# Performance work log

Hardware: AMD Instinct MI355X
Metric: run time of the kernel (lower is better)

The kernel has to match this reference:

```python
import jax, jax.numpy as jnp
import numpy as np

C = 96          # num_features
G = 3           # deform / weight groups
K = 9           # 3x3 kernel taps
OFF_CH = G * 3 * K  # 81: offset-conv output channels


def conv3x3(x, w, b=None):
    out = jax.lax.conv_general_dilated(
        x, w, window_strides=(1, 1), padding=((1, 1), (1, 1)),
        dimension_numbers=('NCHW', 'OIHW', 'NCHW'))
    if b is not None:
        out = out + b[None, :, None, None]
    return out


def offset_gen(x):
    o1, o2, m = jnp.split(x, 3, axis=1)
    return jnp.concatenate([o1, o2], axis=1), jax.nn.sigmoid(m)


def dcn(x, offset, mask, w, b):
    # Modulated deformable conv (DCNv2): offset = [y-offsets (G*K ch), x-offsets (G*K ch)]
    N, Cx, H, W = x.shape
    Cg = Cx // G
    GK = G * K
    dy = offset[:, :GK].reshape(N, G, K, H, W)
    dx = offset[:, GK:].reshape(N, G, K, H, W)
    m = mask.reshape(N, G, K, H, W)
    ky = (jnp.arange(K) // 3 - 1).astype(x.dtype)
    kx = (jnp.arange(K) % 3 - 1).astype(x.dtype)
    # sampling positions: p = p0 + kernel_offset + learned_offset (stride 1, pad 1)
    py = dy + jnp.arange(H, dtype=x.dtype)[:, None] + ky[:, None, None]   # [N,G,K,H,W]
    px = dx + jnp.arange(W, dtype=x.dtype) + kx[:, None, None]
    y0 = jnp.floor(py)
    x0 = jnp.floor(px)
    xf = x.reshape(N, G, Cg, H * W)
    gather = jax.vmap(jax.vmap(lambda xg, ig: xg[:, ig]))  # ([Cg,HW],[KHW]) -> [Cg,KHW]
    val = jnp.zeros((N, G, Cg, K, H, W), x.dtype)
    for cy, cx in ((y0, x0), (y0, x0 + 1), (y0 + 1, x0), (y0 + 1, x0 + 1)):
        wgt = (1 - jnp.abs(py - cy)) * (1 - jnp.abs(px - cx))
        valid = (cy >= 0) & (cy <= H - 1) & (cx >= 0) & (cx <= W - 1)
        iy = jnp.clip(cy, 0, H - 1).astype(jnp.int32)
        ix = jnp.clip(cx, 0, W - 1).astype(jnp.int32)
        idx = (iy * W + ix).reshape(N, G, K * H * W)
        g = gather(xf, idx).reshape(N, G, Cg, K, H, W)
        val = val + g * (wgt * valid.astype(x.dtype))[:, :, None]
    val = val * m[:, :, None]                       # modulation
    wg = w.reshape(G, Cx // G, Cg, K)               # grouped weight [G, Cout/G, Cin/G, K]
    out = jnp.einsum('ngckhw,gock->ngohw', val, wg).reshape(N, Cx, H, W)
    return out + b[None, :, None, None]


def setup_inputs() -> dict:
    key = jax.random.key(0)
    ks = jax.random.split(key, 16)
    B, H, W = 2, 128, 128
    d = {
        'X1': jax.random.normal(ks[0], (B, C, H, W), jnp.float32),
        'X2': jax.random.normal(ks[1], (B, C, H, W), jnp.float32),
        'w_bot': jax.random.normal(ks[2], (C, 2 * C, 3, 3), jnp.float32) * 0.02,
    }
    for i in range(4):
        d[f'w_off{i+1}'] = jax.random.normal(ks[3 + i], (OFF_CH, C, 3, 3), jnp.float32) * 0.02
        d[f'w_d{i+1}'] = jax.random.normal(ks[7 + i], (C, C // G, 3, 3), jnp.float32) * 0.05
        d[f'b_d{i+1}'] = jax.random.normal(ks[11 + i], (C,), jnp.float32) * 0.01
    return d


def reference(X1, X2, w_bot, w_off1, w_off2, w_off3, w_off4,
              w_d1, b_d1, w_d2, b_d2, w_d3, b_d3, w_d4, b_d4):
    B, Cx, H, W = X1.shape
    # frames: f0 = cat(X1, X1), f1 = cat(X1, X2) along channels, flattened to (B*2, 2C, H, W)
    feat = jnp.stack([jnp.concatenate([X1, X1], axis=1),
                      jnp.concatenate([X1, X2], axis=1)], axis=1)
    feat = feat.reshape(B * 2, 2 * Cx, H, W)
    feat = conv3x3(feat, w_bot)
    for w_off, w_d, b_d in ((w_off1, w_d1, b_d1), (w_off2, w_d2, b_d2),
                            (w_off3, w_d3, b_d3), (w_off4, w_d4, b_d4)):
        off, m = offset_gen(conv3x3(feat, w_off))
        feat = dcn(feat, off, m, w_d, b_d)
    return feat[1:2]


if __name__ == '__main__':
    out = reference(**setup_inputs())
    print(out.shape)
```

## Files before the change

### kernel.cpp

```cpp
#include <hip/hip_runtime.h>

#define HW 16384
#define W_ 128
#define RSB 130

typedef short short8 __attribute__((ext_vector_type(8)));
typedef float f32x4 __attribute__((ext_vector_type(4)));
typedef unsigned short ushort8v __attribute__((ext_vector_type(8)));

__device__ __forceinline__ float b2f(unsigned short u) {
    return __uint_as_float(((unsigned)u) << 16);
}
__device__ __forceinline__ unsigned short f2b(float f) {
    unsigned u = __float_as_uint(f);
    return (unsigned short)((u + 0x7fffu + ((u >> 16) & 1u)) >> 16);
}

__global__ __launch_bounds__(256) void pack_nhwc(const float* __restrict__ X1,
                                                 const float* __restrict__ X2,
                                                 unsigned short* __restrict__ dst) {
    int i = blockIdx.x * 256 + threadIdx.x;
    int p = i & (HW - 1);
    int cb = i >> 14;
    if (cb >= 24) return;
    int ch = cb * 8;
    int y = p >> 7, x = p & 127;
    ushort8v o;
#pragma unroll
    for (int j = 0; j < 8; ++j) {
        int c = ch + j;
        float v = (c < 96) ? X1[c * HW + p] : X2[(c - 96) * HW + p];
        o[j] = f2b(v);
    }
    *(ushort8v*)(dst + (size_t)((y + 1) * RSB + (x + 1)) * 192 + ch) = o;
}

__global__ __launch_bounds__(256) void prep_all(
    const float* __restrict__ w_bot,
    const float* __restrict__ w_off0, const float* __restrict__ w_off1,
    const float* __restrict__ w_off2, const float* __restrict__ w_off3,
    const float* __restrict__ w_d0, const float* __restrict__ w_d1,
    const float* __restrict__ w_d2, const float* __restrict__ w_d3,
    unsigned short* __restrict__ wBbot, unsigned short* __restrict__ wBoff,
    unsigned short* __restrict__ wdB,  unsigned short* __restrict__ in_nhwc,
    unsigned short* __restrict__ featA, unsigned short* __restrict__ featB) {
    const int region = blockIdx.y;
    const int i = blockIdx.x * 256 + threadIdx.x;
    if (region == 0) {
        if (i >= 165888) return;
        int v = i & 7, lane = (i >> 3) & 63, t = i >> 9;
        int kc = t % 6; t /= 6;
        int tap = t % 9, nt = t / 9;
        int oc = nt * 16 + (lane & 15), cin = kc * 32 + (lane >> 4) * 8 + v;
        wBbot[i] = f2b(oc < 96 ? w_bot[(oc * 192 + cin) * 9 + tap] : 0.f);
    } else if (region <= 4) {
        if (i >= 82944) return;
        const float* w = region == 1 ? w_off0 : region == 2 ? w_off1
                       : region == 3 ? w_off2 : w_off3;
        int v = i & 7, lane = (i >> 3) & 63, t = i >> 9;
        int kc = t % 3; t /= 3;
        int tap = t % 9, nt = t / 9;
        int oc = nt * 16 + (lane & 15), cin = kc * 32 + (lane >> 4) * 8 + v;
        wBoff[(region - 1) * 82944 + i] = f2b(oc < 81 ? w[(oc * 96 + cin) * 9 + tap] : 0.f);
    } else if (region <= 8) {
        if (i >= 27648) return;
        const float* w = region == 5 ? w_d0 : region == 6 ? w_d1
                       : region == 7 ? w_d2 : w_d3;
        int v = i & 7, lane = (i >> 3) & 63, t = i >> 9;
        int nt = t & 1; t >>= 1;
        int tap = t % 9, g = t / 9;
        int oc = nt * 16 + (lane & 15), c = (lane >> 4) * 8 + v;
        wdB[(region - 5) * 27648 + i] = f2b(w[((g * 32 + oc) * 32 + c) * 9 + tap]);
    } else {
        if (i >= 516 * 48) return;
        int bp = i / 48, c8 = i % 48;
        int y, x;
        if (bp < 130)      { y = 0;   x = bp; }
        else if (bp < 260) { y = 129; x = bp - 130; }
        else { int t2 = bp - 260; y = 1 + (t2 >> 1); x = (t2 & 1) ? 129 : 0; }
        size_t pix = (size_t)y * RSB + x;
        ushort8v z = {0, 0, 0, 0, 0, 0, 0, 0};
        if (c8 < 24)      *(ushort8v*)(in_nhwc + pix * 192 + c8 * 8) = z;
        else if (c8 < 36) *(ushort8v*)(featA + pix * 96 + (c8 - 24) * 8) = z;
        else              *(ushort8v*)(featB + pix * 96 + (c8 - 36) * 8) = z;
    }
}

template<int KC, bool FLAT_OUT>
__global__ __launch_bounds__(256) void conv_mfma(const unsigned short* __restrict__ in,
                                                 const unsigned short* __restrict__ wB,
                                                 unsigned short* __restrict__ outb) {
    const int CP = KC * 32;
    const int tid = threadIdx.x;
    const int lane = tid & 63;
    const int wid = tid >> 6;
    const int msub = wid & 1, nh = wid >> 1;
    const int pbase = blockIdx.x * 32 + msub * 16;
    const int p = pbase + (lane & 15);
    const int y = p >> 7, x = p & 127;
    const int klane = lane >> 4;
    const unsigned short* arow = in + (size_t)((y + 1) * RSB + (x + 1)) * CP + klane * 8;
    const unsigned short* wb = wB + (size_t)(nh * 3) * 9 * KC * 512 + lane * 8;

    f32x4 acc0 = {0.f, 0.f, 0.f, 0.f};
    f32x4 acc1 = {0.f, 0.f, 0.f, 0.f};
    f32x4 acc2 = {0.f, 0.f, 0.f, 0.f};

#pragma unroll
    for (int tap = 0; tap < 9; ++tap) {
        const unsigned short* at = arow + ((tap / 3 - 1) * RSB + (tap % 3 - 1)) * CP;
#pragma unroll
        for (int kc = 0; kc < KC; ++kc) {
            short8 a  = *(const short8*)(at + kc * 32);
            short8 b0 = *(const short8*)(wb + ((0 * 9 + tap) * KC + kc) * 512);
            short8 b1 = *(const short8*)(wb + ((1 * 9 + tap) * KC + kc) * 512);
            short8 b2 = *(const short8*)(wb + ((2 * 9 + tap) * KC + kc) * 512);
            acc0 = __builtin_amdgcn_mfma_f32_16x16x32_bf16(a, b0, acc0, 0, 0, 0);
            acc1 = __builtin_amdgcn_mfma_f32_16x16x32_bf16(a, b1, acc1, 0, 0, 0);
            acc2 = __builtin_amdgcn_mfma_f32_16x16x32_bf16(a, b2, acc2, 0, 0, 0);
        }
    }

    const int col = lane & 15;
#pragma unroll
    for (int r = 0; r < 4; ++r) {
        int pr = pbase + klane * 4 + r;
        int yy = pr >> 7, xx = pr & 127;
        size_t base = FLAT_OUT ? (size_t)pr * 96
                               : (size_t)((yy + 1) * RSB + (xx + 1)) * 96;
        outb[base + (nh * 3 + 0) * 16 + col] = f2b(acc0[r]);
        outb[base + (nh * 3 + 1) * 16 + col] = f2b(acc1[r]);
        outb[base + (nh * 3 + 2) * 16 + col] = f2b(acc2[r]);
    }
}

__global__ __launch_bounds__(256) void dcn_kernel(const unsigned short* __restrict__ feat,
                                                  const unsigned short* __restrict__ offb,
                                                  const unsigned short* __restrict__ wdB,
                                                  const float* __restrict__ b_d,
                                                  void* __restrict__ outp,
                                                  int last) {
    const int tid = threadIdx.x;
    const int lane = tid & 63;
    const int wv = tid >> 6;
    const int g = blockIdx.y;
    const int pb = ((blockIdx.x & 7) << 5) + (blockIdx.x >> 3);
    const int pbase = pb * 64 + wv * 16;
    const int col = lane & 15, klane = lane >> 4;
    const int p = pbase + col;
    const int y = p >> 7, x = p & 127;
    const int coct = klane * 8;

    const unsigned short* orow = offb + (size_t)p * 96 + g * 9;
    float dyv[9], dxv[9], mrv[9];
#pragma unroll
    for (int k = 0; k < 9; ++k) {
        dyv[k] = b2f(orow[k]);
        dxv[k] = b2f(orow[27 + k]);
        mrv[k] = b2f(orow[54 + k]);
    }

    const unsigned short* fgc = feat + g * 32 + coct;
    const unsigned short* wb = wdB + (size_t)g * 9 * 2 * 512 + lane * 8;

    f32x4 acc0 = {0.f, 0.f, 0.f, 0.f};
    f32x4 acc1 = {0.f, 0.f, 0.f, 0.f};

#pragma unroll
    for (int k = 0; k < 9; ++k) {
        float m = 1.f / (1.f + __expf(-mrv[k]));

        float py = dyv[k] + (float)y + (float)(k / 3 - 1);
        float px = dxv[k] + (float)x + (float)(k % 3 - 1);
        float y0f = floorf(py), x0f = floorf(px);
        float fy = py - y0f, fx = px - x0f;

        float vy0 = (y0f >= 0.f   && y0f <= 127.f) ? 1.f : 0.f;
        float vy1 = (y0f >= -1.f  && y0f <= 126.f) ? 1.f : 0.f;
        float vx0 = (x0f >= 0.f   && x0f <= 127.f) ? 1.f : 0.f;
        float vx1 = (x0f >= -1.f  && x0f <= 126.f) ? 1.f : 0.f;

        int iy0r = (int)y0f, ix0r = (int)x0f;
        int iy0 = min(max(iy0r, 0), 127);
        int iy1 = min(max(iy0r + 1, 0), 127);
        int ix0 = min(max(ix0r, 0), 127);
        int ix1 = min(max(ix0r + 1, 0), 127);

        float w00 = (1.f - fy) * (1.f - fx) * vy0 * vx0 * m;
        float w01 = (1.f - fy) * fx        * vy0 * vx1 * m;
        float w10 = fy        * (1.f - fx) * vy1 * vx0 * m;
        float w11 = fy        * fx         * vy1 * vx1 * m;

        int r00 = (iy0 + 1) * RSB + ix0 + 1, r01 = (iy0 + 1) * RSB + ix1 + 1;
        int r10 = (iy1 + 1) * RSB + ix0 + 1, r11 = (iy1 + 1) * RSB + ix1 + 1;
        ushort8v v00 = *(const ushort8v*)(fgc + (size_t)r00 * 96);
        ushort8v v01 = *(const ushort8v*)(fgc + (size_t)r01 * 96);
        ushort8v v10 = *(const ushort8v*)(fgc + (size_t)r10 * 96);
        ushort8v v11 = *(const ushort8v*)(fgc + (size_t)r11 * 96);

        short8 a;
#pragma unroll
        for (int j = 0; j < 8; ++j) {
            float val = w00 * b2f(v00[j]) + w01 * b2f(v01[j])
                      + w10 * b2f(v10[j]) + w11 * b2f(v11[j]);
            a[j] = (short)f2b(val);
        }
        short8 b0 = *(const short8*)(wb + (k * 2 + 0) * 512);
        short8 b1 = *(const short8*)(wb + (k * 2 + 1) * 512);
        acc0 = __builtin_amdgcn_mfma_f32_16x16x32_bf16(a, b0, acc0, 0, 0, 0);
        acc1 = __builtin_amdgcn_mfma_f32_16x16x32_bf16(a, b1, acc1, 0, 0, 0);
    }

#pragma unroll
    for (int r = 0; r < 4; ++r) {
        int pr = pbase + klane * 4 + r;
        int ch0 = g * 32 + col, ch1 = g * 32 + 16 + col;
        float o0 = acc0[r] + b_d[ch0];
        float o1 = acc1[r] + b_d[ch1];
        if (!last) {
            int yy = pr >> 7, xx = pr & 127;
            unsigned short* fo = (unsigned short*)outp;
            size_t base = (size_t)((yy + 1) * RSB + (xx + 1)) * 96;
            fo[base + ch0] = f2b(o0);
            fo[base + ch1] = f2b(o1);
        } else {
            float* fo = (float*)outp;
            fo[(size_t)ch0 * HW + pr] = o0;
            fo[(size_t)ch1 * HW + pr] = o1;
        }
    }
}

extern "C" void kernel_launch(void* const* d_in, const int* in_sizes, int n_in,
                              void* d_out, int out_size, void* d_ws, size_t ws_size,
                              hipStream_t stream) {
    const float* X1    = (const float*)d_in[0];
    const float* X2    = (const float*)d_in[1];
    const float* w_bot = (const float*)d_in[2];
    const float* w_off[4] = {(const float*)d_in[3], (const float*)d_in[6],
                             (const float*)d_in[9], (const float*)d_in[12]};
    const float* w_d[4]   = {(const float*)d_in[4], (const float*)d_in[7],
                             (const float*)d_in[10], (const float*)d_in[13]};
    const float* b_d[4]   = {(const float*)d_in[5], (const float*)d_in[8],
                             (const float*)d_in[11], (const float*)d_in[14]};

    unsigned short* in_nhwc = (unsigned short*)d_ws;
    unsigned short* featA   = in_nhwc + 3244800;
    unsigned short* featB   = featA + 1622400;
    unsigned short* off_b   = featB + 1622400;
    unsigned short* wBbot   = off_b + 1572864;
    unsigned short* wBoff   = wBbot + 165888;
    unsigned short* wdB     = wBoff + 4 * 82944;

    prep_all<<<dim3(648, 10), 256, 0, stream>>>(
        w_bot, w_off[0], w_off[1], w_off[2], w_off[3],
        w_d[0], w_d[1], w_d[2], w_d[3],
        wBbot, wBoff, wdB, in_nhwc, featA, featB);
    pack_nhwc<<<1536, 256, 0, stream>>>(X1, X2, in_nhwc);
    conv_mfma<6, false><<<512, 256, 0, stream>>>(in_nhwc, wBbot, featA);

    unsigned short* cur = featA;
    unsigned short* nxt = featB;
    for (int it = 0; it < 4; ++it) {
        conv_mfma<3, true><<<512, 256, 0, stream>>>(cur, wBoff + it * 82944, off_b);
        void* outp = (it == 3) ? d_out : (void*)nxt;
        dcn_kernel<<<dim3(256, 3), 256, 0, stream>>>(cur, off_b, wdB + it * 27648,
                                                     b_d[it], outp, it == 3 ? 1 : 0);
        unsigned short* t = cur; cur = nxt; nxt = t;
    }
}
```

Baseline: 144.0 us.

## Fuse offset convolution into deformable conv kernel via shared memory

Merges the per-iteration offset/mask 3x3 convolution into the DCN kernel: each 512-thread block first computes 81 offset channels for its 64 pixels with MFMA into LDS, then performs the deformable sampling and grouped conv for all three groups. This removes one kernel launch per iteration and the global round-trip of the bf16 offset buffer, and keeps offsets in fp32. In exchange, the grid shrinks from 768 to 256 blocks and the 12 DCN sub-tasks are unevenly split across 8 waves, reducing parallelism.

```diff
diff --git a/kernel.cpp b/kernel.cpp
--- a/kernel.cpp
+++ b/kernel.cpp
@@ -134,99 +134,138 @@
     }
 }
 
-__global__ __launch_bounds__(256) void dcn_kernel(const unsigned short* __restrict__ feat,
-                                                  const unsigned short* __restrict__ offb,
-                                                  const unsigned short* __restrict__ wdB,
-                                                  const float* __restrict__ b_d,
-                                                  void* __restrict__ outp,
-                                                  int last) {
+__global__ __launch_bounds__(512) void offdcn_kernel(
+    const unsigned short* __restrict__ feat,
+    const unsigned short* __restrict__ wBoff,
+    const unsigned short* __restrict__ wdB,
+    const float* __restrict__ b_d,
+    void* __restrict__ outp, int last) {
+    __shared__ float s_off[64][97];
+
     const int tid = threadIdx.x;
     const int lane = tid & 63;
-    const int wv = tid >> 6;
-    const int g = blockIdx.y;
+    const int w = tid >> 6;
+    const int col = lane & 15, klane = lane >> 4;
     const int pb = ((blockIdx.x & 7) << 5) + (blockIdx.x >> 3);
-    const int pbase = pb * 64 + wv * 16;
-    const int col = lane & 15, klane = lane >> 4;
-    const int p = pbase + col;
-    const int y = p >> 7, x = p & 127;
-    const int coct = klane * 8;
-
-    const unsigned short* orow = offb + (size_t)p * 96 + g * 9;
-    float dyv[9], dxv[9], mrv[9];
-#pragma unroll
-    for (int k = 0; k < 9; ++k) {
-        dyv[k] = b2f(orow[k]);
-        dxv[k] = b2f(orow[27 + k]);
-        mrv[k] = b2f(orow[54 + k]);
-    }
-
-    const unsigned short* fgc = feat + g * 32 + coct;
-    const unsigned short* wb = wdB + (size_t)g * 9 * 2 * 512 + lane * 8;
-
-    f32x4 acc0 = {0.f, 0.f, 0.f, 0.f};
-    f32x4 acc1 = {0.f, 0.f, 0.f, 0.f};
-
-#pragma unroll
-    for (int k = 0; k < 9; ++k) {
-        float m = 1.f / (1.f + __expf(-mrv[k]));
-
-        float py = dyv[k] + (float)y + (float)(k / 3 - 1);
-        float px = dxv[k] + (float)x + (float)(k % 3 - 1);
-        float y0f = floorf(py), x0f = floorf(px);
-        float fy = py - y0f, fx = px - x0f;
-
-        float vy0 = (y0f >= 0.f   && y0f <= 127.f) ? 1.f : 0.f;
-        float vy1 = (y0f >= -1.f  && y0f <= 126.f) ? 1.f : 0.f;
-        float vx0 = (x0f >= 0.f   && x0f <= 127.f) ? 1.f : 0.f;
-        float vx1 = (x0f >= -1.f  && x0f <= 126.f) ? 1.f : 0.f;
-
-        int iy0r = (int)y0f, ix0r = (int)x0f;
-        int iy0 = min(max(iy0r, 0), 127);
-        int iy1 = min(max(iy0r + 1, 0), 127);
-        int ix0 = min(max(ix0r, 0), 127);
-        int ix1 = min(max(ix0r + 1, 0), 127);
-
-        float w00 = (1.f - fy) * (1.f - fx) * vy0 * vx0 * m;
-        float w01 = (1.f - fy) * fx        * vy0 * vx1 * m;
-        float w10 = fy        * (1.f - fx) * vy1 * vx0 * m;
-        float w11 = fy        * fx         * vy1 * vx1 * m;
-
-        int r00 = (iy0 + 1) * RSB + ix0 + 1, r01 = (iy0 + 1) * RSB + ix1 + 1;
-        int r10 = (iy1 + 1) * RSB + ix0 + 1, r11 = (iy1 + 1) * RSB + ix1 + 1;
-        ushort8v v00 = *(const ushort8v*)(fgc + (size_t)r00 * 96);
-        ushort8v v01 = *(const ushort8v*)(fgc + (size_t)r01 * 96);
-        ushort8v v10 = *(const ushort8v*)(fgc + (size_t)r10 * 96);
-        ushort8v v11 = *(const ushort8v*)(fgc + (size_t)r11 * 96);
-
-        short8 a;
-#pragma unroll
-        for (int j = 0; j < 8; ++j) {
-            float val = w00 * b2f(v00[j]) + w01 * b2f(v01[j])
-                      + w10 * b2f(v10[j]) + w11 * b2f(v11[j]);
-            a[j] = (short)f2b(val);
-        }
-        short8 b0 = *(const short8*)(wb + (k * 2 + 0) * 512);
-        short8 b1 = *(const short8*)(wb + (k * 2 + 1) * 512);
-        acc0 = __builtin_amdgcn_mfma_f32_16x16x32_bf16(a, b0, acc0, 0, 0, 0);
-        acc1 = __builtin_amdgcn_mfma_f32_16x16x32_bf16(a, b1, acc1, 0, 0, 0);
-    }
-
-#pragma unroll
-    for (int r = 0; r < 4; ++r) {
-        int pr = pbase + klane * 4 + r;
-        int ch0 = g * 32 + col, ch1 = g * 32 + 16 + col;
-        float o0 = acc0[r] + b_d[ch0];
-        float o1 = acc1[r] + b_d[ch1];
-        if (!last) {
-            int yy = pr >> 7, xx = pr & 127;
-            unsigned short* fo = (unsigned short*)outp;
-            size_t base = (size_t)((yy + 1) * RSB + (xx + 1)) * 96;
-            fo[base + ch0] = f2b(o0);
-            fo[base + ch1] = f2b(o1);
-        } else {
-            float* fo = (float*)outp;
-            fo[(size_t)ch0 * HW + pr] = o0;
-            fo[(size_t)ch1 * HW + pr] = o1;
+    const int P0 = pb * 64;
+
+    {
+        const int pf = w >> 1, nh = w & 1;
+        const int p = P0 + pf * 16 + col;
+        const int y = p >> 7, x = p & 127;
+        const unsigned short* arow = feat + (size_t)((y + 1) * RSB + (x + 1)) * 96 + klane * 8;
+        const unsigned short* wb = wBoff + (size_t)(nh * 3) * 9 * 3 * 512 + lane * 8;
+
+        f32x4 a0 = {0.f, 0.f, 0.f, 0.f};
+        f32x4 a1 = {0.f, 0.f, 0.f, 0.f};
+        f32x4 a2 = {0.f, 0.f, 0.f, 0.f};
+#pragma unroll
+        for (int tap = 0; tap < 9; ++tap) {
+            const unsigned short* at = arow + ((tap / 3 - 1) * RSB + (tap % 3 - 1)) * 96;
+#pragma unroll
+            for (int kc = 0; kc < 3; ++kc) {
+                short8 a  = *(const short8*)(at + kc * 32);
+                short8 b0 = *(const short8*)(wb + ((0 * 9 + tap) * 3 + kc) * 512);
+                short8 b1 = *(const short8*)(wb + ((1 * 9 + tap) * 3 + kc) * 512);
+                short8 b2 = *(const short8*)(wb + ((2 * 9 + tap) * 3 + kc) * 512);
+                a0 = __builtin_amdgcn_mfma_f32_16x16x32_bf16(a, b0, a0, 0, 0, 0);
+                a1 = __builtin_amdgcn_mfma_f32_16x16x32_bf16(a, b1, a1, 0, 0, 0);
+                a2 = __builtin_amdgcn_mfma_f32_16x16x32_bf16(a, b2, a2, 0, 0, 0);
+            }
+        }
+#pragma unroll
+        for (int r = 0; r < 4; ++r) {
+            int pl = pf * 16 + klane * 4 + r;
+            s_off[pl][nh * 48 + 0 * 16 + col] = a0[r];
+            s_off[pl][nh * 48 + 1 * 16 + col] = a1[r];
+            s_off[pl][nh * 48 + 2 * 16 + col] = a2[r];
+        }
+    }
+    __syncthreads();
+
+    for (int sidx = w; sidx < 12; sidx += 8) {
+        const int pf = sidx & 3, g = sidx >> 2;
+        const int p = P0 + pf * 16 + col;
+        const int y = p >> 7, x = p & 127;
+        const int pl = pf * 16 + col;
+        const int coct = klane * 8;
+
+        float dyv[9], dxv[9], mrv[9];
+#pragma unroll
+        for (int k = 0; k < 9; ++k) {
+            dyv[k] = s_off[pl][g * 9 + k];
+            dxv[k] = s_off[pl][27 + g * 9 + k];
+            mrv[k] = s_off[pl][54 + g * 9 + k];
+        }
+
+        const unsigned short* fgc = feat + g * 32 + coct;
+        const unsigned short* wb = wdB + (size_t)g * 9 * 2 * 512 + lane * 8;
+
+        f32x4 acc0 = {0.f, 0.f, 0.f, 0.f};
+        f32x4 acc1 = {0.f, 0.f, 0.f, 0.f};
+
+#pragma unroll
+        for (int k = 0; k < 9; ++k) {
+            float m = 1.f / (1.f + __expf(-mrv[k]));
+
+            float py = dyv[k] + (float)y + (float)(k / 3 - 1);
+            float px = dxv[k] + (float)x + (float)(k % 3 - 1);
+            float y0f = floorf(py), x0f = floorf(px);
+            float fy = py - y0f, fx = px - x0f;
+
+            float vy0 = (y0f >= 0.f   && y0f <= 127.f) ? 1.f : 0.f;
+            float vy1 = (y0f >= -1.f  && y0f <= 126.f) ? 1.f : 0.f;
+            float vx0 = (x0f >= 0.f   && x0f <= 127.f) ? 1.f : 0.f;
+            float vx1 = (x0f >= -1.f  && x0f <= 126.f) ? 1.f : 0.f;
+
+            int iy0r = (int)y0f, ix0r = (int)x0f;
+            int iy0 = min(max(iy0r, 0), 127);
+            int iy1 = min(max(iy0r + 1, 0), 127);
+            int ix0 = min(max(ix0r, 0), 127);
+            int ix1 = min(max(ix0r + 1, 0), 127);
+
+            float w00 = (1.f - fy) * (1.f - fx) * vy0 * vx0 * m;
+            float w01 = (1.f - fy) * fx        * vy0 * vx1 * m;
+            float w10 = fy        * (1.f - fx) * vy1 * vx0 * m;
+            float w11 = fy        * fx         * vy1 * vx1 * m;
+
+            int r00 = (iy0 + 1) * RSB + ix0 + 1, r01 = (iy0 + 1) * RSB + ix1 + 1;
+            int r10 = (iy1 + 1) * RSB + ix0 + 1, r11 = (iy1 + 1) * RSB + ix1 + 1;
+            ushort8v v00 = *(const ushort8v*)(fgc + (size_t)r00 * 96);
+            ushort8v v01 = *(const ushort8v*)(fgc + (size_t)r01 * 96);
+            ushort8v v10 = *(const ushort8v*)(fgc + (size_t)r10 * 96);
+            ushort8v v11 = *(const ushort8v*)(fgc + (size_t)r11 * 96);
+
+            short8 a;
+#pragma unroll
+            for (int j = 0; j < 8; ++j) {
+                float val = w00 * b2f(v00[j]) + w01 * b2f(v01[j])
+                          + w10 * b2f(v10[j]) + w11 * b2f(v11[j]);
+                a[j] = (short)f2b(val);
+            }
+            short8 b0 = *(const short8*)(wb + (k * 2 + 0) * 512);
+            short8 b1 = *(const short8*)(wb + (k * 2 + 1) * 512);
+            acc0 = __builtin_amdgcn_mfma_f32_16x16x32_bf16(a, b0, acc0, 0, 0, 0);
+            acc1 = __builtin_amdgcn_mfma_f32_16x16x32_bf16(a, b1, acc1, 0, 0, 0);
+        }
+
+#pragma unroll
+        for (int r = 0; r < 4; ++r) {
+            int pr = P0 + pf * 16 + klane * 4 + r;
+            int ch0 = g * 32 + col, ch1 = g * 32 + 16 + col;
+            float o0 = acc0[r] + b_d[ch0];
+            float o1 = acc1[r] + b_d[ch1];
+            if (!last) {
+                int yy = pr >> 7, xx = pr & 127;
+                unsigned short* fo = (unsigned short*)outp;
+                size_t base = (size_t)((yy + 1) * RSB + (xx + 1)) * 96;
+                fo[base + ch0] = f2b(o0);
+                fo[base + ch1] = f2b(o1);
+            } else {
+                float* fo = (float*)outp;
+                fo[(size_t)ch0 * HW + pr] = o0;
+                fo[(size_t)ch1 * HW + pr] = o1;
+            }
         }
     }
 }
@@ -247,8 +286,7 @@
     unsigned short* in_nhwc = (unsigned short*)d_ws;
     unsigned short* featA   = in_nhwc + 3244800;
     unsigned short* featB   = featA + 1622400;
-    unsigned short* off_b   = featB + 1622400;
-    unsigned short* wBbot   = off_b + 1572864;
+    unsigned short* wBbot   = featB + 1622400;
     unsigned short* wBoff   = wBbot + 165888;
     unsigned short* wdB     = wBoff + 4 * 82944;
 
@@ -262,10 +300,10 @@
     unsigned short* cur = featA;
     unsigned short* nxt = featB;
     for (int it = 0; it < 4; ++it) {
-        conv_mfma<3, true><<<512, 256, 0, stream>>>(cur, wBoff + it * 82944, off_b);
         void* outp = (it == 3) ? d_out : (void*)nxt;
-        dcn_kernel<<<dim3(256, 3), 256, 0, stream>>>(cur, off_b, wdB + it * 27648,
-                                                     b_d[it], outp, it == 3 ? 1 : 0);
+        offdcn_kernel<<<256, 512, 0, stream>>>(cur, wBoff + it * 82944,
+                                               wdB + it * 27648, b_d[it],
+                                               outp, it == 3 ? 1 : 0);
         unsigned short* t = cur; cur = nxt; nxt = t;
     }
 }
```

Measured after the change: 122.9 us. -14.7%, faster.
